# Performance work log

Measured on AMD Instinct MI355X. Metric: run time of the kernel, lower is better.

## Reference

```python
import jax, jax.numpy as jnp
import numpy as np
import math

D_MODEL = 512
N_HEADS = 8
MAX_SPAN = 512
SPAN_LOSS_COEF = 2e-4
NEG_INF = -1.0e9
R_SIZE = 4.0


def soft_span_mask(span, max_span, seq_len):
    # span: (H,) clamped span fractions
    i_idx = jnp.arange(seq_len, dtype=span.dtype)[:, None]
    j_idx = jnp.arange(seq_len, dtype=span.dtype)[None, :]
    dist = i_idx - j_idx                                  # (T, T)
    eff_span = (span * max_span)[:, None, None]           # (H, 1, 1)
    x = eff_span - dist[None, :, :]                       # (H, T, T)
    R = jnp.clip((x + 1.0) / R_SIZE, 0.0, 1.0)
    causal_ok = dist[None, :, :] >= 0
    log_R = jnp.maximum(jnp.log(R + 1e-10), NEG_INF)
    return jnp.where(causal_ok & (R > 0), log_R, NEG_INF)  # (H, T, T)


def setup_inputs() -> dict:
    key = jax.random.key(0)
    ks = jax.random.split(key, 6)
    B, T, D = 4, 2048, D_MODEL
    w_scale = 0.02
    return {
        "x": jax.random.normal(ks[0], (B, T, D), dtype=jnp.float32),
        "wq": jax.random.normal(ks[1], (D, D), dtype=jnp.float32) * w_scale,
        "wk": jax.random.normal(ks[2], (D, D), dtype=jnp.float32) * w_scale,
        "wv": jax.random.normal(ks[3], (D, D), dtype=jnp.float32) * w_scale,
        "wo": jax.random.normal(ks[4], (D, D), dtype=jnp.float32) * w_scale,
        "span_params": jax.random.uniform(ks[5], (N_HEADS,), dtype=jnp.float32),
    }


def reference(x, wq, wk, wv, wo, span_params):
    B, T, D = x.shape
    H = N_HEADS
    d_h = D // H

    clamped_span = jnp.clip(span_params, 0.0, 1.0)

    # nn.Linear(bias=False): y = x @ W.T
    Q = (x @ wq.T).reshape(B, T, H, d_h).transpose(0, 2, 1, 3)  # (B,H,T,dh)
    K = (x @ wk.T).reshape(B, T, H, d_h).transpose(0, 2, 1, 3)
    V = (x @ wv.T).reshape(B, T, H, d_h).transpose(0, 2, 1, 3)

    scale = 1.0 / math.sqrt(d_h)
    scores = jnp.einsum("bhqd,bhkd->bhqk", Q, K) * scale        # (B,H,T,T)
    scores = scores + soft_span_mask(clamped_span, MAX_SPAN, T)[None]

    weights = jax.nn.softmax(scores, axis=-1)
    out = jnp.einsum("bhqk,bhkd->bhqd", weights, V)             # (B,H,T,dh)
    out = out.transpose(0, 2, 1, 3).reshape(B, T, D)
    output = out @ wo.T

    span_loss = SPAN_LOSS_COEF * clamped_span.mean()
    return output, span_loss
```

## Files before the change

kernel.cpp:

```cpp
#include <hip/hip_runtime.h>
#include <math.h>

#define T_SEQ   2048
#define DMODEL  512
#define NHEADS  8
#define DH      64
#define NEG_INF -1.0e9f

typedef __attribute__((ext_vector_type(8))) short short8;
typedef __attribute__((ext_vector_type(4))) float f32x4;
typedef unsigned int u32;
typedef unsigned short u16;

__device__ __forceinline__ u16 f2bf(float f) {
    union { float f; u32 u; } w; w.f = f;
    return (u16)((w.u + 0x8000u) >> 16);
}

__device__ __forceinline__ u32 cvt_pk_bf16(float lo, float hi) {
    u32 r;
    asm("v_cvt_pk_bf16_f32 %0, %1, %2" : "=v"(r) : "v"(lo), "v"(hi));
    return r;
}

__device__ __forceinline__ void async_load16(const u16* g, u16* l) {
    __builtin_amdgcn_global_load_lds(
        (const __attribute__((address_space(1))) u32*)(const void*)g,
        (__attribute__((address_space(3))) u32*)(void*)l, 16, 0, 0);
}

__global__ void cast_all(const float* __restrict__ x,  const float* __restrict__ wq,
                         const float* __restrict__ wk, const float* __restrict__ wv,
                         const float* __restrict__ wo, const float* __restrict__ sp,
                         u16* __restrict__ xb,  u16* __restrict__ wqb,
                         u16* __restrict__ wkb, u16* __restrict__ wvb,
                         u16* __restrict__ wob, float* __restrict__ loss_out)
{
    const int bid = blockIdx.x;
    const float* src; u16* dst; int i;
    if (bid < 4096) { src = x; dst = xb; i = bid * 256 + threadIdx.x; }
    else {
        const int wsel = (bid - 4096) >> 8;
        src = (wsel == 0) ? wq : (wsel == 1) ? wk : (wsel == 2) ? wv : wo;
        dst = (wsel == 0) ? wqb : (wsel == 1) ? wkb : (wsel == 2) ? wvb : wob;
        i = ((bid - 4096) & 255) * 256 + threadIdx.x;
    }
    float4 v = ((const float4*)src)[i];
    ushort4 o;
    o.x = f2bf(v.x); o.y = f2bf(v.y); o.z = f2bf(v.z); o.w = f2bf(v.w);
    ((ushort4*)dst)[i] = o;
    if (bid == 5119 && threadIdx.x == 0) {
        float s = 0.0f;
        for (int h = 0; h < NHEADS; ++h)
            s += fminf(fmaxf(sp[h], 0.0f), 1.0f);
        loss_out[0] = 2e-4f * (s * 0.125f);
    }
}

__global__ __launch_bounds__(256)
void gemm_bf16(const u16* __restrict__ A,
               const u16* __restrict__ W0, const u16* __restrict__ W1,
               const u16* __restrict__ W2,
               u16* __restrict__ Cb0, u16* __restrict__ Cb1,
               u16* __restrict__ Cb2,
               float* __restrict__ Cf, int scatter)
{
    constexpr int K = 512, BK = 64;
    const u16* W  = (blockIdx.z == 0) ? W0 : (blockIdx.z == 1) ? W1 : W2;
    u16*       Cb = (blockIdx.z == 0) ? Cb0 : (blockIdx.z == 1) ? Cb1 : Cb2;

    __shared__ __align__(16) u16 smem[16384];
    u16* As = smem;
    u16* Bs = smem + 8192;

    const int t    = threadIdx.x;
    const int lane = t & 63;
    const int wave = t >> 6;
    const int wm   = wave >> 1, wn = wave & 1;
    const int m0   = blockIdx.x * 128, n0 = blockIdx.y * 128;

    const int srow = t >> 3;
    const int kb   = (t & 7) ^ (srow & 7);
    const u16* gA = A + (size_t)(m0 + srow) * K + kb * 8;
    const u16* gW = W + (size_t)(n0 + srow) * K + kb * 8;

    const int rA = wm * 64 + (lane & 15);
    const int rB = wn * 64 + (lane & 15);
    const int kq = lane >> 4;
    const int offA0 = rA * BK + ((kq      ^ (rA & 7)) * 8);
    const int offA1 = rA * BK + (((4 + kq) ^ (rA & 7)) * 8);
    const int offB0 = rB * BK + ((kq      ^ (rB & 7)) * 8);
    const int offB1 = rB * BK + (((4 + kq) ^ (rB & 7)) * 8);

    f32x4 acc[4][4];
#pragma unroll
    for (int it = 0; it < 4; ++it)
#pragma unroll
        for (int jt = 0; jt < 4; ++jt) acc[it][jt] = (f32x4)0.0f;

    for (int k0 = 0; k0 < K; k0 += BK) {
        __syncthreads();
#pragma unroll
        for (int i = 0; i < 4; ++i) {
            async_load16(gA + k0 + i * (32 * K), As + t * 8 + i * 2048);
            async_load16(gW + k0 + i * (32 * K), Bs + t * 8 + i * 2048);
        }
        __syncthreads();

        short8 af[4][2], bfr[4][2];
#pragma unroll
        for (int it = 0; it < 4; ++it) {
            af[it][0]  = *(const short8*)(As + offA0 + it * 16 * BK);
            af[it][1]  = *(const short8*)(As + offA1 + it * 16 * BK);
            bfr[it][0] = *(const short8*)(Bs + offB0 + it * 16 * BK);
            bfr[it][1] = *(const short8*)(Bs + offB1 + it * 16 * BK);
        }
#pragma unroll
        for (int it = 0; it < 4; ++it)
#pragma unroll
            for (int jt = 0; jt < 4; ++jt) {
                acc[it][jt] = __builtin_amdgcn_mfma_f32_16x16x32_bf16(
                    af[it][0], bfr[jt][0], acc[it][jt], 0, 0, 0);
                acc[it][jt] = __builtin_amdgcn_mfma_f32_16x16x32_bf16(
                    af[it][1], bfr[jt][1], acc[it][jt], 0, 0, 0);
            }
    }

    const int r0 = (lane >> 4) * 4;
    const int cl = lane & 15;

    if (scatter) {
        constexpr int P = 136;
#pragma unroll
        for (int rnd = 0; rnd < 2; ++rnd) {
            __syncthreads();
#pragma unroll
            for (int s = 0; s < 2; ++s) {
                const int it = rnd * 2 + s;
                const int lrow = wm * 32 + s * 16 + r0;
#pragma unroll
                for (int jt = 0; jt < 4; ++jt) {
                    const int cc = wn * 64 + jt * 16 + cl;
#pragma unroll
                    for (int r = 0; r < 4; ++r)
                        smem[(lrow + r) * P + cc] = f2bf(acc[it][jt][r]);
                }
            }
            __syncthreads();
            const int lrow2 = t >> 2;
            const int h2    = (t >> 1) & 1;
            const int dhalf = t & 1;
            const int grow  = m0 + (lrow2 >> 5) * 64 + rnd * 32 + (lrow2 & 31);
            const int b     = grow >> 11, tt = grow & 2047;
            const int h     = (n0 >> 6) + h2;
            u16* dst = Cb + ((size_t)((b * NHEADS + h) * T_SEQ + tt)) * DH + dhalf * 32;
            const u16* srcl = smem + lrow2 * P + h2 * 64 + dhalf * 32;
#pragma unroll
            for (int i = 0; i < 4; ++i)
                ((uint4*)dst)[i] = *(const uint4*)(srcl + i * 8);
        }
    } else {
#pragma unroll
        for (int it = 0; it < 4; ++it) {
#pragma unroll
            for (int r = 0; r < 4; ++r) {
                const int row = m0 + wm * 64 + it * 16 + r0 + r;
#pragma unroll
                for (int jt = 0; jt < 4; ++jt) {
                    const int col = n0 + wn * 64 + jt * 16 + cl;
                    Cf[(size_t)row * DMODEL + col] = acc[it][jt][r];
                }
            }
        }
    }
}

__global__ __launch_bounds__(256)
void transpose_v(const u16* __restrict__ V, u16* __restrict__ Vt)
{
    __shared__ u16 tile[64][72];
    const int bh = blockIdx.y;
    const int j0 = blockIdx.x * 64;
    const u16* src = V + (size_t)bh * (T_SEQ * DH) + (size_t)j0 * DH;
    u16* dst = Vt + (size_t)bh * (T_SEQ * DH) + j0;
    const int t = threadIdx.x;
    const int jr = t >> 2, c0 = (t & 3) * 16;
    uint4 a = *(const uint4*)(src + (size_t)jr * DH + c0);
    uint4 b = *(const uint4*)(src + (size_t)jr * DH + c0 + 8);
    *(uint4*)&tile[jr][c0]     = a;
    *(uint4*)&tile[jr][c0 + 8] = b;
    __syncthreads();
    const int d = t >> 2, jc = (t & 3) * 16;
    union { uint4 v; u16 s[8]; } pa, pb;
#pragma unroll
    for (int i = 0; i < 8; ++i) pa.s[i] = tile[jc + i][d];
#pragma unroll
    for (int i = 0; i < 8; ++i) pb.s[i] = tile[jc + 8 + i][d];
    *(uint4*)(dst + (size_t)d * T_SEQ + jc)     = pa.v;
    *(uint4*)(dst + (size_t)d * T_SEQ + jc + 8) = pb.v;
}

__global__ __launch_bounds__(128)
void attn_mfma(const u16* __restrict__ Q, const u16* __restrict__ K,
               const u16* __restrict__ Vt, const float* __restrict__ span_params,
               u16* __restrict__ out)
{
    __shared__ __align__(16) u16 Ks[64 * 64];
    __shared__ __align__(16) u16 Vs[64 * 64];
    __shared__ __align__(16) u16 Ps[2][1024];

    const int tid  = threadIdx.x;
    const int lane = tid & 63;
    const int w    = tid >> 6;
    const int nl   = lane & 15;
    const int quad = lane >> 4;
    const int swz  = (nl & 7) << 3;

    const int l  = blockIdx.x;
    const int k  = l >> 8;
    const int c  = l & 255;
    const int h  = k;
    const int b  = c >> 6;
    const int qb = ((c & 63) + 8 * k) & 63;
    const int bh = b * 8 + h;
    const int i0 = qb * 32;
    const int q0 = i0 + w * 16;

    const u16* Qh = Q  + (size_t)bh * (T_SEQ * DH);
    const u16* Kh = K  + (size_t)bh * (T_SEQ * DH);
    const u16* Vh = Vt + (size_t)bh * (DH * T_SEQ);

    float span = span_params[h];
    span = fminf(fmaxf(span, 0.0f), 1.0f);
    const float eff_span = span * 512.0f;
    const int wspan = (int)(eff_span + 1.0f) + 1;

    const float SCL = 0.125f * 1.44269504f;

    short8 qf0 = *(const short8*)(Qh + (size_t)(q0 + nl) * DH + quad * 8);
    short8 qf1 = *(const short8*)(Qh + (size_t)(q0 + nl) * DH + 32 + quad * 8);

    const int srow = tid >> 3;
    const int sg   = (tid & 7) ^ (srow & 7);
    const u16* gK = Kh + (size_t)srow * DH + sg * 8;
    const u16* gV = Vh + (size_t)srow * T_SEQ + sg * 8;

    f32x4 o[4];
    float m_r = -1.0e30f, l_r = 0.0f;
#pragma unroll
    for (int d = 0; d < 4; ++d) o[d] = (f32x4)0.0f;

    int j_lo = i0 - wspan;
    if (j_lo < 0) j_lo = 0;
    j_lo &= ~63;

    u16* Psw = Ps[w];

    for (int j0 = j_lo; j0 <= i0 + 31; j0 += 64) {
        __syncthreads();
#pragma unroll
        for (int i = 0; i < 4; ++i) {
            async_load16(gK + (size_t)(j0 + i * 16) * DH, Ks + tid * 8 + i * 1024);
            async_load16(gV + j0 + (size_t)(i * 16) * T_SEQ, Vs + tid * 8 + i * 1024);
        }
        __syncthreads();

        f32x4 s[4];
        bool any[4];
        __builtin_amdgcn_s_setprio(1);
#pragma unroll
        for (int n = 0; n < 4; ++n) {
            const int jn = j0 + n * 16;
            any[n] = (jn <= q0 + 15) &&
                     ((float)(q0 - jn - 15) < eff_span + 1.0f);
            s[n] = (f32x4)0.0f;
            if (any[n]) {
                const int row = n * 16 + nl;
                const u16* kp = Ks + row * 64;
                short8 b0 = *(const short8*)(kp + ((quad ^ (row & 7)) * 8));
                short8 b1 = *(const short8*)(kp + (((4 + quad) ^ (row & 7)) * 8));
                s[n] = __builtin_amdgcn_mfma_f32_16x16x32_bf16(b0, qf0, s[n], 0, 0, 0);
                s[n] = __builtin_amdgcn_mfma_f32_16x16x32_bf16(b1, qf1, s[n], 0, 0, 0);
            }
        }
        __builtin_amdgcn_s_setprio(0);

        const int qg = q0 + nl;
        float tmax = -1.0e30f;
#pragma unroll
        for (int n = 0; n < 4; ++n) {
            if (!any[n]) continue;
            const int jn = j0 + n * 16;
            const int jb = jn + quad * 4;
            const bool causal_b = (jn + 15 > q0);
            const bool span_b   = ((float)(q0 + 15 - jn) > eff_span - 3.0f);
            if (!causal_b && !span_b) {
#pragma unroll
                for (int r = 0; r < 4; ++r) {
                    const float sv = s[n][r] * SCL;
                    s[n][r] = sv;
                    tmax = fmaxf(tmax, sv);
                }
            } else if (!span_b) {
#pragma unroll
                for (int r = 0; r < 4; ++r) {
                    const int dist = qg - (jb + r);
                    const float sv = (dist >= 0) ? s[n][r] * SCL : NEG_INF;
                    s[n][r] = sv;
                    tmax = fmaxf(tmax, sv);
                }
            } else {
#pragma unroll
                for (int r = 0; r < 4; ++r) {
                    const int dist = qg - (jb + r);
                    float sv = NEG_INF;
                    if (dist >= 0) {
                        float xv = eff_span - (float)dist;
                        float R  = fminf(fmaxf((xv + 1.0f) * 0.25f, 0.0f), 1.0f);
                        if (R > 0.0f)
                            sv = s[n][r] * SCL +
                                 ((R < 1.0f) ? __log2f(R + 1e-10f) : 0.0f);
                    }
                    s[n][r] = sv;
                    tmax = fmaxf(tmax, sv);
                }
            }
        }

        float t2 = fmaxf(tmax, __shfl_xor(tmax, 16));
        t2 = fmaxf(t2, __shfl_xor(t2, 32));
        const float m_new = fmaxf(m_r, t2);
        const float alpha = exp2f(m_r - m_new);
        m_r = m_new;

        float psum = 0.0f;
#pragma unroll
        for (int n = 0; n < 4; ++n) {
            u32 w0 = 0, w1 = 0;
            if (any[n]) {
                const float p0 = exp2f(s[n][0] - m_r);
                const float p1 = exp2f(s[n][1] - m_r);
                const float p2 = exp2f(s[n][2] - m_r);
                const float p3 = exp2f(s[n][3] - m_r);
                psum += (p0 + p1) + (p2 + p3);
                w0 = cvt_pk_bf16(p0, p1);
                w1 = cvt_pk_bf16(p2, p3);
            }
            uint2 wv; wv.x = w0; wv.y = w1;
            *(uint2*)&Psw[nl * 64 + ((n * 16 + quad * 4) ^ swz)] = wv;
        }
        float ps = psum + __shfl_xor(psum, 16);
        ps += __shfl_xor(ps, 32);
        l_r = l_r * alpha + ps;
#pragma unroll
        for (int d = 0; d < 4; ++d)
#pragma unroll
            for (int r = 0; r < 4; ++r) o[d][r] *= alpha;

        const bool kf0 = any[0] | any[1];
        const bool kf1 = any[2] | any[3];
        short8 pa0 = *(const short8*)&Psw[nl * 64 + ((quad * 8) ^ swz)];
        short8 pa1 = *(const short8*)&Psw[nl * 64 + ((32 + quad * 8) ^ swz)];
        __builtin_amdgcn_s_setprio(1);
#pragma unroll
        for (int d = 0; d < 4; ++d) {
            const int vrow = d * 16 + nl;
            const u16* vp = Vs + vrow * 64;
            if (kf0) {
                short8 vb0 = *(const short8*)(vp + ((quad ^ (vrow & 7)) * 8));
                o[d] = __builtin_amdgcn_mfma_f32_16x16x32_bf16(vb0, pa0, o[d], 0, 0, 0);
            }
            if (kf1) {
                short8 vb1 = *(const short8*)(vp + (((4 + quad) ^ (vrow & 7)) * 8));
                o[d] = __builtin_amdgcn_mfma_f32_16x16x32_bf16(vb1, pa1, o[d], 0, 0, 0);
            }
        }
        __builtin_amdgcn_s_setprio(0);
    }

    const float inv_l = 1.0f / l_r;
    u16* op = out + (size_t)(b * T_SEQ + q0 + nl) * DMODEL + h * 64 + quad * 4;
#pragma unroll
    for (int d = 0; d < 4; ++d) {
        uint2 wv;
        wv.x = cvt_pk_bf16(o[d][0] * inv_l, o[d][1] * inv_l);
        wv.y = cvt_pk_bf16(o[d][2] * inv_l, o[d][3] * inv_l);
        *(uint2*)(op + d * 16) = wv;
    }
}

extern "C" void kernel_launch(void* const* d_in, const int* in_sizes, int n_in,
                              void* d_out, int out_size, void* d_ws, size_t ws_size,
                              hipStream_t stream)
{
    (void)in_sizes; (void)n_in; (void)out_size; (void)ws_size;
    const float* x  = (const float*)d_in[0];
    const float* wq = (const float*)d_in[1];
    const float* wk = (const float*)d_in[2];
    const float* wv = (const float*)d_in[3];
    const float* wo = (const float*)d_in[4];
    const float* sp = (const float*)d_in[5];
    float* out = (float*)d_out;

    const size_t elems = (size_t)4 * T_SEQ * DMODEL;
    u16* xb  = (u16*)d_ws;
    u16* Qb  = xb  + elems;
    u16* Kb  = Qb  + elems;
    u16* Vb  = Kb  + elems;
    u16* Vtb = Vb  + elems;
    u16* Ab  = Vtb + elems;
    u16* wqb = Ab  + elems;
    u16* wkb = wqb + 262144;
    u16* wvb = wkb + 262144;
    u16* wob = wvb + 262144;

    cast_all<<<5120, 256, 0, stream>>>(x, wq, wk, wv, wo, sp,
                                       xb, wqb, wkb, wvb, wob, out + elems);
    gemm_bf16<<<dim3(64, 4, 3), 256, 0, stream>>>(
        xb, wqb, wkb, wvb, Qb, Kb, Vb, nullptr, 1);
    transpose_v<<<dim3(32, 32), 256, 0, stream>>>(Vb, Vtb);
    attn_mfma<<<dim3(2048), 128, 0, stream>>>(Qb, Kb, Vtb, sp, Ab);
    gemm_bf16<<<dim3(64, 4, 1), 256, 0, stream>>>(
        Ab, wob, wob, wob, nullptr, nullptr, nullptr, out, 0);
}
```

Baseline: 149.8 us.

## Prefetch next K/V tile into registers to overlap global loads with compute

Replaces the direct global-to-LDS async loads in the attention loop with a register-staged software pipeline. The next tile's K/V is loaded into registers while the current tile is computed, then written to LDS at the top of the next iteration. Raw s_barrier plus explicit waitcnts replace __syncthreads, and launch bounds now request 4 blocks per CU. This hides global load latency but adds register pressure and LDS write instructions.

```diff
diff --git a/kernel.cpp b/kernel.cpp
--- a/kernel.cpp
+++ b/kernel.cpp
@@ -27,6 +27,12 @@
     __builtin_amdgcn_global_load_lds(
         (const __attribute__((address_space(1))) u32*)(const void*)g,
         (__attribute__((address_space(3))) u32*)(void*)l, 16, 0, 0);
+}
+
+__device__ __forceinline__ void barrier_raw() {
+    __builtin_amdgcn_sched_barrier(0);
+    asm volatile("s_barrier" ::: "memory");
+    __builtin_amdgcn_sched_barrier(0);
 }
 
 __global__ void cast_all(const float* __restrict__ x,  const float* __restrict__ wq,
@@ -200,7 +206,17 @@
     *(uint4*)(dst + (size_t)d * T_SEQ + jc + 8) = pb.v;
 }
 
-__global__ __launch_bounds__(128)
+__device__ __forceinline__ void load_kv_regs(const u16* gK, const u16* gV, int jj,
+                                             uint4* kreg, uint4* vreg)
+{
+#pragma unroll
+    for (int i = 0; i < 4; ++i) {
+        kreg[i] = *(const uint4*)(gK + (size_t)(jj + i * 16) * DH);
+        vreg[i] = *(const uint4*)(gV + jj + (size_t)(i * 16) * T_SEQ);
+    }
+}
+
+__global__ __launch_bounds__(128, 4)
 void attn_mfma(const u16* __restrict__ Q, const u16* __restrict__ K,
                const u16* __restrict__ Vt, const float* __restrict__ span_params,
                u16* __restrict__ out)
@@ -253,17 +269,27 @@
     int j_lo = i0 - wspan;
     if (j_lo < 0) j_lo = 0;
     j_lo &= ~63;
+    const int ntiles = ((i0 + 31 - j_lo) >> 6) + 1;
 
     u16* Psw = Ps[w];
 
-    for (int j0 = j_lo; j0 <= i0 + 31; j0 += 64) {
-        __syncthreads();
+    uint4 kreg[4], vreg[4];
+    load_kv_regs(gK, gV, j_lo, kreg, vreg);
+
+    for (int t = 0; t < ntiles; ++t) {
+        const int j0 = j_lo + (t << 6);
+
+        asm volatile("s_waitcnt vmcnt(0)" ::: "memory");
+        barrier_raw();
 #pragma unroll
         for (int i = 0; i < 4; ++i) {
-            async_load16(gK + (size_t)(j0 + i * 16) * DH, Ks + tid * 8 + i * 1024);
-            async_load16(gV + j0 + (size_t)(i * 16) * T_SEQ, Vs + tid * 8 + i * 1024);
-        }
-        __syncthreads();
+            *(uint4*)(Ks + tid * 8 + i * 1024) = kreg[i];
+            *(uint4*)(Vs + tid * 8 + i * 1024) = vreg[i];
+        }
+        if (t + 1 < ntiles)
+            load_kv_regs(gK, gV, j0 + 64, kreg, vreg);
+        asm volatile("s_waitcnt lgkmcnt(0)" ::: "memory");
+        barrier_raw();
 
         f32x4 s[4];
         bool any[4];
```

After: 205.2 us. 1.37x slower.

## Double-buffer K/V tiles with async LDS loads and shrink key tile to 32

Applied to the files above, without the earlier changes.

Replaces the single-buffered 64-key K/V staging with a two-buffer pipeline of 32-key tiles. The next tile is prefetched asynchronously while the current one is computed, using explicit vmcnt waits and raw barriers in place of __syncthreads. The aim is to hide global-load latency and trim masked work at span edges through finer tile granularity. The cost is more loop iterations with two barriers each, and correctness now depends on the hand-written waitcnt and barrier placement.

```diff
diff --git a/kernel.cpp b/kernel.cpp
--- a/kernel.cpp
+++ b/kernel.cpp
@@ -27,6 +27,12 @@
     __builtin_amdgcn_global_load_lds(
         (const __attribute__((address_space(1))) u32*)(const void*)g,
         (__attribute__((address_space(3))) u32*)(void*)l, 16, 0, 0);
+}
+
+__device__ __forceinline__ void barrier_raw() {
+    __builtin_amdgcn_sched_barrier(0);
+    asm volatile("s_barrier" ::: "memory");
+    __builtin_amdgcn_sched_barrier(0);
 }
 
 __global__ void cast_all(const float* __restrict__ x,  const float* __restrict__ wq,
@@ -205,9 +211,9 @@
                const u16* __restrict__ Vt, const float* __restrict__ span_params,
                u16* __restrict__ out)
 {
-    __shared__ __align__(16) u16 Ks[64 * 64];
-    __shared__ __align__(16) u16 Vs[64 * 64];
-    __shared__ __align__(16) u16 Ps[2][1024];
+    __shared__ __align__(16) u16 Ks[2][32 * 64];
+    __shared__ __align__(16) u16 Vs[2][64 * 32];
+    __shared__ __align__(16) u16 Ps[2][16 * 64];
 
     const int tid  = threadIdx.x;
     const int lane = tid & 63;
@@ -217,11 +223,11 @@
     const int swz  = (nl & 7) << 3;
 
     const int l  = blockIdx.x;
-    const int k  = l >> 8;
+    const int kk = l >> 8;
     const int c  = l & 255;
-    const int h  = k;
+    const int h  = kk;
     const int b  = c >> 6;
-    const int qb = ((c & 63) + 8 * k) & 63;
+    const int qb = ((c & 63) + 8 * kk) & 63;
     const int bh = b * 8 + h;
     const int i0 = qb * 32;
     const int q0 = i0 + w * 16;
@@ -240,10 +246,19 @@
     short8 qf0 = *(const short8*)(Qh + (size_t)(q0 + nl) * DH + quad * 8);
     short8 qf1 = *(const short8*)(Qh + (size_t)(q0 + nl) * DH + 32 + quad * 8);
 
-    const int srow = tid >> 3;
-    const int sg   = (tid & 7) ^ (srow & 7);
-    const u16* gK = Kh + (size_t)srow * DH + sg * 8;
-    const u16* gV = Vh + (size_t)srow * T_SEQ + sg * 8;
+    const int srowK = tid >> 3;
+    const int sgK   = (tid & 7) ^ (srowK & 7);
+    const u16* gK = Kh + (size_t)srowK * DH + sgK * 8;
+    const int srowV = tid >> 2;
+    const int sgV   = (tid & 3) ^ (srowV & 3);
+    const u16* gV = Vh + (size_t)srowV * T_SEQ + sgV * 8;
+
+#define STAGE_KV(bi, jj) do {                                                    \
+        async_load16(gK + (size_t)(jj) * DH,              Ks[bi] + tid * 8);         \
+        async_load16(gK + (size_t)((jj) + 16) * DH,       Ks[bi] + tid * 8 + 1024);  \
+        async_load16(gV + (jj),                           Vs[bi] + tid * 8);         \
+        async_load16(gV + (size_t)32 * T_SEQ + (jj),      Vs[bi] + tid * 8 + 1024);  \
+    } while (0)
 
     f32x4 o[4];
     float m_r = -1.0e30f, l_r = 0.0f;
@@ -252,31 +267,40 @@
 
     int j_lo = i0 - wspan;
     if (j_lo < 0) j_lo = 0;
-    j_lo &= ~63;
+    j_lo &= ~31;
+    const int nt = ((i0 + 31 - j_lo) >> 5) + 1;
 
     u16* Psw = Ps[w];
 
-    for (int j0 = j_lo; j0 <= i0 + 31; j0 += 64) {
-        __syncthreads();
-#pragma unroll
-        for (int i = 0; i < 4; ++i) {
-            async_load16(gK + (size_t)(j0 + i * 16) * DH, Ks + tid * 8 + i * 1024);
-            async_load16(gV + j0 + (size_t)(i * 16) * T_SEQ, Vs + tid * 8 + i * 1024);
-        }
-        __syncthreads();
-
-        f32x4 s[4];
-        bool any[4];
+    STAGE_KV(0, j_lo);
+    int buf = 0;
+
+    for (int t = 0; t < nt; ++t) {
+        const int j0 = j_lo + (t << 5);
+
+        if (t + 1 < nt) {
+            STAGE_KV(buf ^ 1, j0 + 32);
+            asm volatile("s_waitcnt vmcnt(4)" ::: "memory");
+        } else {
+            asm volatile("s_waitcnt vmcnt(0)" ::: "memory");
+        }
+        barrier_raw();
+
+        const u16* Kb = Ks[buf];
+        const u16* Vb = Vs[buf];
+
+        f32x4 s[2];
+        bool any[2];
         __builtin_amdgcn_s_setprio(1);
 #pragma unroll
-        for (int n = 0; n < 4; ++n) {
+        for (int n = 0; n < 2; ++n) {
             const int jn = j0 + n * 16;
             any[n] = (jn <= q0 + 15) &&
                      ((float)(q0 - jn - 15) < eff_span + 1.0f);
             s[n] = (f32x4)0.0f;
             if (any[n]) {
                 const int row = n * 16 + nl;
-                const u16* kp = Ks + row * 64;
+                const u16* kp = Kb + row * 64;
                 short8 b0 = *(const short8*)(kp + ((quad ^ (row & 7)) * 8));
                 short8 b1 = *(const short8*)(kp + (((4 + quad) ^ (row & 7)) * 8));
                 s[n] = __builtin_amdgcn_mfma_f32_16x16x32_bf16(b0, qf0, s[n], 0, 0, 0);
@@ -288,7 +312,7 @@
         const int qg = q0 + nl;
         float tmax = -1.0e30f;
 #pragma unroll
-        for (int n = 0; n < 4; ++n) {
+        for (int n = 0; n < 2; ++n) {
             if (!any[n]) continue;
             const int jn = j0 + n * 16;
             const int jb = jn + quad * 4;
@@ -335,7 +359,7 @@
 
         float psum = 0.0f;
 #pragma unroll
-        for (int n = 0; n < 4; ++n) {
+        for (int n = 0; n < 2; ++n) {
             u32 w0 = 0, w1 = 0;
             if (any[n]) {
                 const float p0 = exp2f(s[n][0] - m_r);
@@ -357,26 +381,24 @@
 #pragma unroll
             for (int r = 0; r < 4; ++r) o[d][r] *= alpha;
 
-        const bool kf0 = any[0] | any[1];
-        const bool kf1 = any[2] | any[3];
+        const bool kf = any[0] | any[1];
         short8 pa0 = *(const short8*)&Psw[nl * 64 + ((quad * 8) ^ swz)];
-        short8 pa1 = *(const short8*)&Psw[nl * 64 + ((32 + quad * 8) ^ swz)];
         __builtin_amdgcn_s_setprio(1);
-#pragma unroll
-        for (int d = 0; d < 4; ++d) {
-            const int vrow = d * 16 + nl;
-            const u16* vp = Vs + vrow * 64;
-            if (kf0) {
-                short8 vb0 = *(const short8*)(vp + ((quad ^ (vrow & 7)) * 8));
+        if (kf) {
+#pragma unroll
+            for (int d = 0; d < 4; ++d) {
+                const int vrow = d * 16 + nl;
+                const u16* vp = Vb + vrow * 32;
+                short8 vb0 = *(const short8*)(vp + ((quad ^ (vrow & 3)) * 8));
                 o[d] = __builtin_amdgcn_mfma_f32_16x16x32_bf16(vb0, pa0, o[d], 0, 0, 0);
             }
-            if (kf1) {
-                short8 vb1 = *(const short8*)(vp + (((4 + quad) ^ (vrow & 7)) * 8));
-                o[d] = __builtin_amdgcn_mfma_f32_16x16x32_bf16(vb1, pa1, o[d], 0, 0, 0);
-            }
         }
         __builtin_amdgcn_s_setprio(0);
-    }
+
+        barrier_raw();
+        buf ^= 1;
+    }
+#undef STAGE_KV
 
     const float inv_l = 1.0f / l_r;
     u16* op = out + (size_t)(b * T_SEQ + q0 + nl) * DMODEL + h * 64 + quad * 4;
```

Result: no change. 152.3 us (+1.6%).
